# Kernel tuning notes

Measured on AMD Instinct MI355X. Metric: run time of the kernel, lower is better.

Reference implementation:

```python
import jax, jax.numpy as jnp
import numpy as np

C = 128                      # channels per irrep
LS = [0, 0, 1, 1, 2, 2]      # active irreps (0e,0o,1e,1o,2e,2o), sorted order
D = C * sum(2 * l + 1 for l in LS)  # 2304
N = 100000                   # nodes


def setup_inputs() -> dict:
    key = jax.random.key(0)
    ks = jax.random.split(key, 7)
    inp = {"x": jax.random.normal(ks[0], (N, D), dtype=jnp.float32)}
    scale = 1.0 / np.sqrt(C)
    for name, k in zip(["W0p", "W0m", "W1p", "W1m", "W2p", "W2m"], ks[1:]):
        inp[name] = jax.random.normal(k, (C, C), dtype=jnp.float32) * scale
    return inp


def reference(x, W0p, W0m, W1p, W1m, W2p, W2m):
    # Split flat features into per-(l,parity) blocks [N, C, 2l+1],
    # mix channels per irrep (movedim + Linear in torch == einsum here),
    # merge back and add residual.
    Ws = [W0p, W0m, W1p, W1m, W2p, W2m]
    idx = 0
    parts = []
    for l, W in zip(LS, Ws):
        d = C * (2 * l + 1)
        blk = x[:, idx:idx + d].reshape(-1, C, 2 * l + 1)  # [N, C, m]
        idx += d
        y = jnp.einsum('ncm,dc->ndm', blk, W)              # channel mix per m
        parts.append(y.reshape(-1, d))
    return x + jnp.concatenate(parts, axis=-1)
```

## Files before the change

### kernel.cpp

```cpp
#include <hip/hip_runtime.h>
#include <hip/hip_bf16.h>

typedef float f32x4 __attribute__((ext_vector_type(4)));
typedef short s16x8 __attribute__((ext_vector_type(8)));

__device__ __forceinline__ unsigned short f32_to_bf16(float f){
    union { float f; unsigned u; } v; v.f = f;
    unsigned r = v.u + 0x7fffu + ((v.u >> 16) & 1u);
    return (unsigned short)(r >> 16);
}
__device__ __forceinline__ unsigned pack2(float a, float b){
    float2 t; t.x = a; t.y = b;
    __hip_bfloat162 h = __float22bfloat162_rn(t);
    union { __hip_bfloat162 h; unsigned u; } c; c.h = h;
    return c.u;
}

template<int N> __device__ __forceinline__ void wait_vmcnt(){
    if constexpr (N == 0)       asm volatile("s_waitcnt vmcnt(0)"  ::: "memory");
    else if constexpr (N == 1)  asm volatile("s_waitcnt vmcnt(1)"  ::: "memory");
    else if constexpr (N == 2)  asm volatile("s_waitcnt vmcnt(2)"  ::: "memory");
    else if constexpr (N == 3)  asm volatile("s_waitcnt vmcnt(3)"  ::: "memory");
    else if constexpr (N == 4)  asm volatile("s_waitcnt vmcnt(4)"  ::: "memory");
    else if constexpr (N == 6)  asm volatile("s_waitcnt vmcnt(6)"  ::: "memory");
    else if constexpr (N == 8)  asm volatile("s_waitcnt vmcnt(8)"  ::: "memory");
    else if constexpr (N == 9)  asm volatile("s_waitcnt vmcnt(9)"  ::: "memory");
    else if constexpr (N == 12) asm volatile("s_waitcnt vmcnt(12)" ::: "memory");
    else static_assert(N == 0, "add wait case");
    __builtin_amdgcn_sched_barrier(0);
}

template<int A, int B, int C, int D>
__device__ __forceinline__ void wait_sel(bool first, bool has2){
    if (first) { if (has2) wait_vmcnt<A>(); else wait_vmcnt<B>(); }
    else       { if (has2) wait_vmcnt<C>(); else wait_vmcnt<D>(); }
}

__device__ __forceinline__ void bar_sync(){
    asm volatile("s_waitcnt lgkmcnt(0)" ::: "memory");
    __builtin_amdgcn_s_barrier();
    __builtin_amdgcn_sched_barrier(0);
}

__device__ __forceinline__ void dma16(const float* g, float* l){
    __builtin_amdgcn_global_load_lds(
        (const __attribute__((address_space(1))) unsigned int*)g,
        (__attribute__((address_space(3))) unsigned int*)l, 16, 0, 0);
}

__global__ __launch_bounds__(256)
void wconv_kernel(const float* __restrict__ W0p, const float* __restrict__ W0m,
                  const float* __restrict__ W1p, const float* __restrict__ W1m,
                  const float* __restrict__ W2p, const float* __restrict__ W2m,
                  unsigned short* __restrict__ wbf)
{
    const int idx = blockIdx.x * 256 + threadIdx.x;
    const int w  = idx >> 14;
    const int rc = idx & 16383;
    const float* Wp;
    switch (w) {
        case 0: Wp = W0p; break;  case 1: Wp = W0m; break;
        case 2: Wp = W1p; break;  case 3: Wp = W1m; break;
        case 4: Wp = W2p; break;  default: Wp = W2m; break;
    }
    const float v = Wp[rc] + (((rc >> 7) == (rc & 127)) ? 1.0f : 0.0f);
    wbf[idx] = f32_to_bf16(v);
}

template<int ML>
__device__ __forceinline__
void lx_body(const float* __restrict__ x, const unsigned short* __restrict__ wb,
             float* __restrict__ out, int yoff, int wg, int G, int ntiles,
             char* smem)
{
    constexpr int BLK  = 128 * ML;
    constexpr int NTB  = 4 * BLK;
    constexpr int CH   = NTB / 256;
    constexpr int HI   = CH / 4 + 1;
    constexpr int LO   = CH / 4;
    constexpr int RROWS= 4 * ML;
    constexpr int RTC  = (RROWS + 15) / 16;
    constexpr int LDSS = 136;

    float*          lin  = (float*)smem;
    unsigned short* lbf  = (unsigned short*)(smem + 2*NTB*4);
    float*          lout = (float*)(smem + 2*NTB*4 + RTC*16*LDSS*2);

    const int tid = threadIdx.x;
    const int wv  = tid >> 6, ln = tid & 63;
    const int l16 = ln & 15,  lhi = ln >> 4;

    s16x8 bfr[4][2];
    #pragma unroll
    for (int s = 0; s < 4; ++s)
        #pragma unroll
        for (int tf = 0; tf < 2; ++tf)
            bfr[s][tf] = *reinterpret_cast<const s16x8*>(
                wb + (wv * 32 + tf * 16 + l16) * 128 + s * 32 + lhi * 8);

    auto dma_tile = [&](int t, int cur) {
        const float* gb = x + (size_t)t * 4 * 2304 + yoff;
        float* lb = lin + cur * NTB;
        #pragma unroll
        for (int c = wv; c < CH; c += 4) {
            const int dw = c * 256 + ln * 4;
            const int nl = dw / BLK, r = dw - nl * BLK;
            dma16(gb + (size_t)nl * 2304 + r, lb + c * 256);
        }
    };
    auto flush_tile = [&](int t) {
        float* gb = out + (size_t)t * 4 * 2304 + yoff;
        #pragma unroll
        for (int c = wv; c < CH; c += 4) {
            const int dw = c * 256 + ln * 4;
            const int nl = dw / BLK, r = dw - nl * BLK;
            *reinterpret_cast<float4*>(gb + (size_t)nl * 2304 + r) =
                *reinterpret_cast<const float4*>(&lout[dw]);
        }
    };

    int t = wg, cur = 0;
    bool has1 = (t + G) < ntiles;
    dma_tile(t, 0);
    if (has1) dma_tile(t + G, 1);
    if (wv < 2) { if (has1) wait_vmcnt<HI>(); else wait_vmcnt<0>(); }
    else        { if (has1) wait_vmcnt<LO>(); else wait_vmcnt<0>(); }
    bar_sync();

    bool first = true;
    while (true) {
        {
            const float* sp = lin + cur * NTB + wv * BLK + ln * 2 * ML;
            float v[2 * ML];
            #pragma unroll
            for (int i = 0; i < ML; ++i) {
                const float2 t2 = *reinterpret_cast<const float2*>(sp + i * 2);
                v[i * 2] = t2.x; v[i * 2 + 1] = t2.y;
            }
            #pragma unroll
            for (int mm = 0; mm < ML; ++mm)
                *reinterpret_cast<unsigned*>(&lbf[(wv * ML + mm) * LDSS + ln * 2]) =
                    pack2(v[mm], v[ML + mm]);
        }
        bar_sync();

        const bool has2 = (t + 2 * G) < ntiles;
        if (has2) dma_tile(t + 2 * G, cur);

        f32x4 acc[RTC][2];
        #pragma unroll
        for (int rt = 0; rt < RTC; ++rt) {
            acc[rt][0] = (f32x4){0.f,0.f,0.f,0.f};
            acc[rt][1] = (f32x4){0.f,0.f,0.f,0.f};
        }
        #pragma unroll
        for (int s = 0; s < 4; ++s) {
            const int k0 = s * 32 + lhi * 8;
            #pragma unroll
            for (int rt = 0; rt < RTC; ++rt) {
                const s16x8 af = *reinterpret_cast<const s16x8*>(
                    &lbf[(rt * 16 + l16) * LDSS + k0]);
                acc[rt][0] = __builtin_amdgcn_mfma_f32_16x16x32_bf16(af, bfr[s][0], acc[rt][0], 0, 0, 0);
                acc[rt][1] = __builtin_amdgcn_mfma_f32_16x16x32_bf16(af, bfr[s][1], acc[rt][1], 0, 0, 0);
            }
        }

        #pragma unroll
        for (int rt = 0; rt < RTC; ++rt)
            #pragma unroll
            for (int tf = 0; tf < 2; ++tf) {
                const int col = wv * 32 + tf * 16 + l16;
                #pragma unroll
                for (int j = 0; j < 4; ++j) {
                    const int row = rt * 16 + lhi * 4 + j;
                    if (row < RROWS) {
                        const int nl = row / ML;
                        lout[nl * BLK + col * ML + (row - nl * ML)] = acc[rt][tf][j];
                    }
                }
            }
        bar_sync();

        flush_tile(t);

        has1 = (t + G) < ntiles;
        if (!has1) break;
        if (wv < 2) wait_sel<2*HI, HI, 3*HI, 2*HI>(first, has2);
        else        wait_sel<2*LO, LO, 3*LO, 2*LO>(first, has2);
        bar_sync();
        t += G; cur ^= 1; first = false;
    }
}

__device__ __forceinline__
void l0_body(const float* __restrict__ x, const unsigned short* __restrict__ wbf,
             float* __restrict__ out, int wg, int G, int ntiles, char* smem)
{
    float* lin = (float*)smem;

    const int tid = threadIdx.x;
    const int wv  = tid >> 6, ln = tid & 63;
    const int l16 = ln & 15,  lhi = ln >> 4;
    const int b     = wv >> 1;
    const int dbase = (wv & 1) * 64;
    const unsigned short* wb = wbf + b * 16384;

    s16x8 afr[4][4];
    #pragma unroll
    for (int s = 0; s < 4; ++s)
        #pragma unroll
        for (int dt = 0; dt < 4; ++dt)
            afr[s][dt] = *reinterpret_cast<const s16x8*>(
                wb + (dbase + dt * 16 + l16) * 128 + s * 32 + lhi * 8);

    auto dma_tile = [&](int t, int cur) {
        const float* gb = x + (size_t)t * 16 * 2304;
        float* lb = lin + cur * 4096;
        #pragma unroll
        for (int c = wv; c < 16; c += 4) {
            const int dw = c * 256 + ln * 4;
            const int node = dw >> 8, r = dw & 255;
            dma16(gb + (size_t)node * 2304 + (r ^ ((node & 7) << 2)), lb + c * 256);
        }
    };

    int t = wg, cur = 0;
    bool has1 = (t + G) < ntiles;
    dma_tile(t, 0);
    if (has1) { dma_tile(t + G, 1); wait_vmcnt<4>(); } else wait_vmcnt<0>();
    bar_sync();

    while (true) {
        const bool has2 = (t + 2 * G) < ntiles;

        f32x4 acc[4];
        #pragma unroll
        for (int dt = 0; dt < 4; ++dt) acc[dt] = (f32x4){0.f,0.f,0.f,0.f};

        const float* bp = lin + cur * 4096;
        const int nb = l16 * 256;
        const int sw = (l16 & 7) << 2;
        #pragma unroll
        for (int s = 0; s < 4; ++s) {
            const int c0 = b * 128 + s * 32 + lhi * 8;
            const float4 v0 = *reinterpret_cast<const float4*>(&bp[nb + ((c0    ) ^ sw)]);
            const float4 v1 = *reinterpret_cast<const float4*>(&bp[nb + ((c0 + 4) ^ sw)]);
            union { s16x8 v; unsigned u[4]; } bf;
            bf.u[0] = pack2(v0.x, v0.y); bf.u[1] = pack2(v0.z, v0.w);
            bf.u[2] = pack2(v1.x, v1.y); bf.u[3] = pack2(v1.z, v1.w);
            #pragma unroll
            for (int dt = 0; dt < 4; ++dt)
                acc[dt] = __builtin_amdgcn_mfma_f32_16x16x32_bf16(afr[s][dt], bf.v, acc[dt], 0, 0, 0);
        }
        bar_sync();

        float* dst = out + ((size_t)t * 16 + l16) * 2304 + b * 128 + dbase + lhi * 4;
        #pragma unroll
        for (int dt = 0; dt < 4; ++dt) {
            float4 vv; vv.x = acc[dt][0]; vv.y = acc[dt][1];
                       vv.z = acc[dt][2]; vv.w = acc[dt][3];
            *reinterpret_cast<float4*>(dst + dt * 16) = vv;
        }

        if (has2) dma_tile(t + 2 * G, cur);
        has1 = (t + G) < ntiles;
        if (!has1) break;
        if (has2) wait_vmcnt<8>(); else wait_vmcnt<4>();
        bar_sync();
        t += G; cur ^= 1;
    }
}

#define SMEM_MAX 39424
__global__ __launch_bounds__(256, 4)
void fused_kernel(const float* __restrict__ x, const unsigned short* __restrict__ wbf,
                  float* __restrict__ out, int n4, int n16)
{
    __shared__ __attribute__((aligned(16))) char smem[SMEM_MAX];
    const int b = blockIdx.x;
    if (b < 576) {
        const int p = (b >= 288);
        lx_body<5>(x, wbf + (size_t)(4 + p) * 16384, out,
                   p ? 1664 : 1024, b - p * 288, 288, n4, smem);
    } else if (b < 912) {
        const int bb = b - 576;
        const int p = (bb >= 168);
        lx_body<3>(x, wbf + (size_t)(2 + p) * 16384, out,
                   p ? 640 : 256, bb - p * 168, 168, n4, smem);
    } else {
        l0_body(x, wbf, out, b - 912, 112, n16, smem);
    }
}

extern "C" void kernel_launch(void* const* d_in, const int* in_sizes, int n_in,
                              void* d_out, int out_size, void* d_ws, size_t ws_size,
                              hipStream_t stream) {
    const float* x   = (const float*)d_in[0];
    const float* W0p = (const float*)d_in[1];
    const float* W0m = (const float*)d_in[2];
    const float* W1p = (const float*)d_in[3];
    const float* W1m = (const float*)d_in[4];
    const float* W2p = (const float*)d_in[5];
    const float* W2m = (const float*)d_in[6];
    float* out = (float*)d_out;
    unsigned short* wbf = (unsigned short*)d_ws;

    const int N = in_sizes[0] / 2304;

    wconv_kernel<<<384, 256, 0, stream>>>(W0p, W0m, W1p, W1m, W2p, W2m, wbf);
    fused_kernel<<<1024, 256, 0, stream>>>(x, wbf, out, N / 4, N / 16);
}
```

Before: 393.2 us.

## Fold weight bf16 conversion into main kernel and re-split MFMA work by rows

```diff
diff --git a/kernel.cpp b/kernel.cpp
--- a/kernel.cpp
+++ b/kernel.cpp
@@ -25,7 +25,6 @@
     else if constexpr (N == 6)  asm volatile("s_waitcnt vmcnt(6)"  ::: "memory");
     else if constexpr (N == 8)  asm volatile("s_waitcnt vmcnt(8)"  ::: "memory");
     else if constexpr (N == 9)  asm volatile("s_waitcnt vmcnt(9)"  ::: "memory");
-    else if constexpr (N == 12) asm volatile("s_waitcnt vmcnt(12)" ::: "memory");
     else static_assert(N == 0, "add wait case");
     __builtin_amdgcn_sched_barrier(0);
 }
@@ -48,28 +47,9 @@
         (__attribute__((address_space(3))) unsigned int*)l, 16, 0, 0);
 }
 
-__global__ __launch_bounds__(256)
-void wconv_kernel(const float* __restrict__ W0p, const float* __restrict__ W0m,
-                  const float* __restrict__ W1p, const float* __restrict__ W1m,
-                  const float* __restrict__ W2p, const float* __restrict__ W2m,
-                  unsigned short* __restrict__ wbf)
-{
-    const int idx = blockIdx.x * 256 + threadIdx.x;
-    const int w  = idx >> 14;
-    const int rc = idx & 16383;
-    const float* Wp;
-    switch (w) {
-        case 0: Wp = W0p; break;  case 1: Wp = W0m; break;
-        case 2: Wp = W1p; break;  case 3: Wp = W1m; break;
-        case 4: Wp = W2p; break;  default: Wp = W2m; break;
-    }
-    const float v = Wp[rc] + (((rc >> 7) == (rc & 127)) ? 1.0f : 0.0f);
-    wbf[idx] = f32_to_bf16(v);
-}
-
 template<int ML>
 __device__ __forceinline__
-void lx_body(const float* __restrict__ x, const unsigned short* __restrict__ wb,
+void lx_body(const float* __restrict__ x, const float* __restrict__ W,
              float* __restrict__ out, int yoff, int wg, int G, int ntiles,
              char* smem)
 {
@@ -81,6 +61,8 @@
     constexpr int RROWS= 4 * ML;
     constexpr int RTC  = (RROWS + 15) / 16;
     constexpr int LDSS = 136;
+    constexpr int CG   = (RTC >= 2) ? 2 : 4;
+    constexpr int NTF  = 8 / CG;
 
     float*          lin  = (float*)smem;
     unsigned short* lbf  = (unsigned short*)(smem + 2*NTB*4);
@@ -89,14 +71,27 @@
     const int tid = threadIdx.x;
     const int wv  = tid >> 6, ln = tid & 63;
     const int l16 = ln & 15,  lhi = ln >> 4;
-
-    s16x8 bfr[4][2];
+    const int th  = wv / CG;
+    const int ch  = wv % CG;
+    const int colbase = ch * (NTF * 16);
+
+    s16x8 bfr[4][NTF];
     #pragma unroll
-    for (int s = 0; s < 4; ++s)
-        #pragma unroll
-        for (int tf = 0; tf < 2; ++tf)
-            bfr[s][tf] = *reinterpret_cast<const s16x8*>(
-                wb + (wv * 32 + tf * 16 + l16) * 128 + s * 32 + lhi * 8);
+    for (int s = 0; s < 4; ++s) {
+        const int k0 = s * 32 + lhi * 8;
+        #pragma unroll
+        for (int tf = 0; tf < NTF; ++tf) {
+            const int d = colbase + tf * 16 + l16;
+            const float4 w0 = *reinterpret_cast<const float4*>(W + d * 128 + k0);
+            const float4 w1 = *reinterpret_cast<const float4*>(W + d * 128 + k0 + 4);
+            const float w8[8] = {w0.x,w0.y,w0.z,w0.w,w1.x,w1.y,w1.z,w1.w};
+            union { s16x8 v; unsigned short us[8]; } b;
+            #pragma unroll
+            for (int j = 0; j < 8; ++j)
+                b.us[j] = f32_to_bf16(w8[j] + ((d == k0 + j) ? 1.0f : 0.0f));
+            bfr[s][tf] = b.v;
+        }
+    }
 
     auto dma_tile = [&](int t, int cur) {
         const float* gb = x + (size_t)t * 4 * 2304 + yoff;
@@ -147,38 +142,32 @@
         const bool has2 = (t + 2 * G) < ntiles;
         if (has2) dma_tile(t + 2 * G, cur);
 
-        f32x4 acc[RTC][2];
-        #pragma unroll
-        for (int rt = 0; rt < RTC; ++rt) {
-            acc[rt][0] = (f32x4){0.f,0.f,0.f,0.f};
-            acc[rt][1] = (f32x4){0.f,0.f,0.f,0.f};
-        }
+        f32x4 acc[NTF];
+        #pragma unroll
+        for (int tf = 0; tf < NTF; ++tf) acc[tf] = (f32x4){0.f,0.f,0.f,0.f};
+
         #pragma unroll
         for (int s = 0; s < 4; ++s) {
             const int k0 = s * 32 + lhi * 8;
-            #pragma unroll
-            for (int rt = 0; rt < RTC; ++rt) {
-                const s16x8 af = *reinterpret_cast<const s16x8*>(
-                    &lbf[(rt * 16 + l16) * LDSS + k0]);
-                acc[rt][0] = __builtin_amdgcn_mfma_f32_16x16x32_bf16(af, bfr[s][0], acc[rt][0], 0, 0, 0);
-                acc[rt][1] = __builtin_amdgcn_mfma_f32_16x16x32_bf16(af, bfr[s][1], acc[rt][1], 0, 0, 0);
-            }
-        }
-
-        #pragma unroll
-        for (int rt = 0; rt < RTC; ++rt)
-            #pragma unroll
-            for (int tf = 0; tf < 2; ++tf) {
-                const int col = wv * 32 + tf * 16 + l16;
-                #pragma unroll
-                for (int j = 0; j < 4; ++j) {
-                    const int row = rt * 16 + lhi * 4 + j;
-                    if (row < RROWS) {
-                        const int nl = row / ML;
-                        lout[nl * BLK + col * ML + (row - nl * ML)] = acc[rt][tf][j];
-                    }
+            const s16x8 af = *reinterpret_cast<const s16x8*>(
+                &lbf[(th * 16 + l16) * LDSS + k0]);
+            #pragma unroll
+            for (int tf = 0; tf < NTF; ++tf)
+                acc[tf] = __builtin_amdgcn_mfma_f32_16x16x32_bf16(af, bfr[s][tf], acc[tf], 0, 0, 0);
+        }
+
+        #pragma unroll
+        for (int tf = 0; tf < NTF; ++tf) {
+            const int col = colbase + tf * 16 + l16;
+            #pragma unroll
+            for (int j = 0; j < 4; ++j) {
+                const int row = th * 16 + lhi * 4 + j;
+                if (row < RROWS) {
+                    const int nl = row / ML;
+                    lout[nl * BLK + col * ML + (row - nl * ML)] = acc[tf][j];
                 }
             }
+        }
         bar_sync();
 
         flush_tile(t);
@@ -193,8 +182,9 @@
 }
 
 __device__ __forceinline__
-void l0_body(const float* __restrict__ x, const unsigned short* __restrict__ wbf,
-             float* __restrict__ out, int wg, int G, int ntiles, char* smem)
+void l0_body(const float* __restrict__ x, const float* __restrict__ W0p,
+             const float* __restrict__ W0m, float* __restrict__ out,
+             int wg, int G, int ntiles, char* smem)
 {
     float* lin = (float*)smem;
 
@@ -203,15 +193,25 @@
     const int l16 = ln & 15,  lhi = ln >> 4;
     const int b     = wv >> 1;
     const int dbase = (wv & 1) * 64;
-    const unsigned short* wb = wbf + b * 16384;
+    const float* __restrict__ W = b ? W0m : W0p;
 
     s16x8 afr[4][4];
     #pragma unroll
-    for (int s = 0; s < 4; ++s)
-        #pragma unroll
-        for (int dt = 0; dt < 4; ++dt)
-            afr[s][dt] = *reinterpret_cast<const s16x8*>(
-                wb + (dbase + dt * 16 + l16) * 128 + s * 32 + lhi * 8);
+    for (int s = 0; s < 4; ++s) {
+        const int k0 = s * 32 + lhi * 8;
+        #pragma unroll
+        for (int dt = 0; dt < 4; ++dt) {
+            const int d = dbase + dt * 16 + l16;
+            const float4 w0 = *reinterpret_cast<const float4*>(W + d * 128 + k0);
+            const float4 w1 = *reinterpret_cast<const float4*>(W + d * 128 + k0 + 4);
+            const float w8[8] = {w0.x,w0.y,w0.z,w0.w,w1.x,w1.y,w1.z,w1.w};
+            union { s16x8 v; unsigned short us[8]; } a;
+            #pragma unroll
+            for (int j = 0; j < 8; ++j)
+                a.us[j] = f32_to_bf16(w8[j] + ((d == k0 + j) ? 1.0f : 0.0f));
+            afr[s][dt] = a.v;
+        }
+    }
 
     auto dma_tile = [&](int t, int cur) {
         const float* gb = x + (size_t)t * 16 * 2304;
@@ -273,22 +273,23 @@
 
 #define SMEM_MAX 39424
 __global__ __launch_bounds__(256, 4)
-void fused_kernel(const float* __restrict__ x, const unsigned short* __restrict__ wbf,
+void fused_kernel(const float* __restrict__ x,
+                  const float* __restrict__ W0p, const float* __restrict__ W0m,
+                  const float* __restrict__ W1p, const float* __restrict__ W1m,
+                  const float* __restrict__ W2p, const float* __restrict__ W2m,
                   float* __restrict__ out, int n4, int n16)
 {
     __shared__ __attribute__((aligned(16))) char smem[SMEM_MAX];
     const int b = blockIdx.x;
     if (b < 576) {
         const int p = (b >= 288);
-        lx_body<5>(x, wbf + (size_t)(4 + p) * 16384, out,
-                   p ? 1664 : 1024, b - p * 288, 288, n4, smem);
+        lx_body<5>(x, p ? W2m : W2p, out, p ? 1664 : 1024, b - p * 288, 288, n4, smem);
     } else if (b < 912) {
         const int bb = b - 576;
         const int p = (bb >= 168);
-        lx_body<3>(x, wbf + (size_t)(2 + p) * 16384, out,
-                   p ? 640 : 256, bb - p * 168, 168, n4, smem);
+        lx_body<3>(x, p ? W1m : W1p, out, p ? 640 : 256, bb - p * 168, 168, n4, smem);
     } else {
-        l0_body(x, wbf, out, b - 912, 112, n16, smem);
+        l0_body(x, W0p, W0m, out, b - 912, 112, n16, smem);
     }
 }
 
@@ -303,10 +304,9 @@
     const float* W2p = (const float*)d_in[5];
     const float* W2m = (const float*)d_in[6];
     float* out = (float*)d_out;
-    unsigned short* wbf = (unsigned short*)d_ws;
 
     const int N = in_sizes[0] / 2304;
 
-    wconv_kernel<<<384, 256, 0, stream>>>(W0p, W0m, W1p, W1m, W2p, W2m, wbf);
-    fused_kernel<<<1024, 256, 0, stream>>>(x, wbf, out, N / 4, N / 16);
-}
+    fused_kernel<<<1024, 256, 0, stream>>>(x, W0p, W0m, W1p, W1m, W2p, W2m,
+                                           out, N / 4, N / 16);
+}
```

Result: slower. 411.9 us (+4.7%).
